# Performance work log

Measured on AMD Instinct MI355X. Metric: run time of the kernel, lower is better.

The kernel has to match this reference:

```python
import jax, jax.numpy as jnp
import numpy as np

D_MODEL = 1024
NUM_HEADS = 16
D_KEY = D_MODEL // NUM_HEADS


def setup_inputs() -> dict:
    key = jax.random.key(0)
    ks = jax.random.split(key, 9)
    B, S = 2, 2048
    s = 1.0 / np.sqrt(D_MODEL)
    return {
        "x": jax.random.normal(ks[0], (B, S, D_MODEL), dtype=jnp.float32),
        "W_q": jax.random.normal(ks[1], (D_MODEL, D_MODEL), dtype=jnp.float32) * s,
        "b_q": jnp.zeros((D_MODEL,), dtype=jnp.float32),
        "W_k": jax.random.normal(ks[2], (D_MODEL, D_MODEL), dtype=jnp.float32) * s,
        "b_k": jnp.zeros((D_MODEL,), dtype=jnp.float32),
        "W_v": jax.random.normal(ks[3], (D_MODEL, D_MODEL), dtype=jnp.float32) * s,
        "b_v": jnp.zeros((D_MODEL,), dtype=jnp.float32),
        "W_o": jax.random.normal(ks[4], (D_MODEL, D_MODEL), dtype=jnp.float32) * s,
        "b_o": jnp.zeros((D_MODEL,), dtype=jnp.float32),
    }


def reference(x, W_q, b_q, W_k, b_k, W_v, b_v, W_o, b_o):
    B, S, _ = x.shape
    # Linear projections (torch nn.Linear: x @ W.T + b; here W stored as [in, out])
    Q = x @ W_q + b_q
    K = x @ W_k + b_k
    V = x @ W_v + b_v
    # [B, S, H, dk] -> [B, H, S, dk]
    def split_heads(t):
        return t.reshape(B, S, NUM_HEADS, D_KEY).transpose(0, 2, 1, 3)
    Q, K, V = split_heads(Q), split_heads(K), split_heads(V)
    scale = 1.0 / np.sqrt(D_KEY).astype(np.float32)
    logits = jnp.einsum("bhqd,bhkd->bhqk", Q, K) * scale  # [B,H,S,S]
    weights = jax.nn.softmax(logits, axis=-1)
    ctx = jnp.einsum("bhqk,bhkd->bhqd", weights, V)       # [B,H,S,dk]
    concat = ctx.transpose(0, 2, 1, 3).reshape(B, S, D_MODEL)
    return concat @ W_o + b_o
```

## Files before the change

### kernel.cpp

```cpp
#include <hip/hip_runtime.h>
#include <cstdint>
#include <cstddef>

#define SEQ   2048
#define NH    16
#define DK    64
#define DM    1024
#define MTOT  4096
#define QSCALE (0.125f * 1.44269504088896f)

typedef __attribute__((ext_vector_type(8))) short           short8;
typedef __attribute__((ext_vector_type(8))) unsigned short  ushort8;
typedef __attribute__((ext_vector_type(4))) unsigned short  ushort4v;
typedef __attribute__((ext_vector_type(2))) unsigned int    uint2v;
typedef __attribute__((ext_vector_type(4))) unsigned int    uint4v;
typedef __attribute__((ext_vector_type(4))) float           float4v;
typedef unsigned short u16;
typedef unsigned int   u32;

__device__ inline float4v mfma16(short8 a, short8 b, float4v c) {
    return __builtin_amdgcn_mfma_f32_16x16x32_bf16(a, b, c, 0, 0, 0);
}
__device__ inline u16 f2bf(float f) {
    u32 u = __float_as_uint(f);
    u += 0x7fffu + ((u >> 16) & 1u);
    return (u16)(u >> 16);
}
__device__ inline u32 pkbf(float a, float b) {
    u32 r;
    asm("v_cvt_pk_bf16_f32 %0, %1, %2" : "=v"(r) : "v"(a), "v"(b));
    return r;
}
__device__ inline float ex2(float x) {
    float r;
    asm("v_exp_f32 %0, %1" : "=v"(r) : "v"(x));
    return r;
}
__device__ inline void pl32swap(u32& a, u32& b) {
    asm("v_permlane32_swap_b32 %0, %1" : "+v"(a), "+v"(b));
}
__device__ inline void pl16swap(u32& a, u32& b) {
    asm("v_permlane16_swap_b32 %0, %1" : "+v"(a), "+v"(b));
}
__device__ inline void gld16(const void* g, void* lds) {
    __builtin_amdgcn_global_load_lds(
        (const __attribute__((address_space(1))) u32*)g,
        (__attribute__((address_space(3))) u32*)lds, 16, 0, 0);
}

__global__ __launch_bounds__(256)
void prep(const float* __restrict__ x, u16* __restrict__ xb,
          const float* __restrict__ W0, const float* __restrict__ W1,
          const float* __restrict__ W2, const float* __restrict__ W3,
          u16* __restrict__ T0, u16* __restrict__ T1,
          u16* __restrict__ T2, u16* __restrict__ T3)
{
    __shared__ u16 t[64][68];
    if (blockIdx.x < 2048) {
        const int i = blockIdx.x * 256 + threadIdx.x;
        const float4v a = ((const float4v*)x)[2 * i];
        const float4v b = ((const float4v*)x)[2 * i + 1];
        ushort8 o;
        #pragma unroll
        for (int j = 0; j < 4; j++) { o[j] = f2bf(a[j]); o[4 + j] = f2bf(b[j]); }
        ((ushort8*)xb)[i] = o;
        return;
    }
    const int bi = blockIdx.x - 2048;
    const int bx = bi & 15, by = (bi >> 4) & 15, bz = bi >> 8;
    const float* W; u16* T;
    switch (bz) {
        case 0: W = W0; T = T0; break;
        case 1: W = W1; T = T1; break;
        case 2: W = W2; T = T2; break;
        default: W = W3; T = T3; break;
    }
    const int n0 = bx * 64, k0 = by * 64;
    const int r  = threadIdx.x >> 4;
    const int c4 = (threadIdx.x & 15) * 4;
    #pragma unroll
    for (int i = 0; i < 4; i++) {
        float4v v = *(const float4v*)&W[(size_t)(k0 + r + i * 16) * DM + n0 + c4];
        #pragma unroll
        for (int j = 0; j < 4; j++) t[r + i * 16][c4 + j] = f2bf(v[j]);
    }
    __syncthreads();
    #pragma unroll
    for (int i = 0; i < 4; i++) {
        const int rr = r + i * 16;
        ushort4v o;
        #pragma unroll
        for (int j = 0; j < 4; j++) o[j] = t[c4 + j][rr];
        *(ushort4v*)&T[(size_t)(n0 + rr) * DM + k0 + c4] = o;
    }
}

template<int TM, int BN, int MODE>
__global__ __launch_bounds__(512)
void gemm_bt(const u16* __restrict__ A, const u16* __restrict__ WT,
             const float* __restrict__ bq, const float* __restrict__ bk,
             const float* __restrict__ bv,
             void* __restrict__ out0, u16* __restrict__ outK, u16* __restrict__ outV)
{
    constexpr int NT = 512;
    constexpr int MF = TM / 32;
    constexpr int NF = BN / 64;
    __shared__ u16 Al[2][TM][64];
    __shared__ u16 Bl[2][BN][64];
    const int tid  = threadIdx.x;
    const int lane = tid & 63, w = tid >> 6;
    const int quad = lane >> 4, l16 = lane & 15;

    const int nxb  = gridDim.x;
    const int wgid = blockIdx.y * nxb + blockIdx.x;
    const int per  = (nxb * gridDim.y) >> 3;
    const int nl   = (wgid & 7) * per + (wgid >> 3);
    const int n0 = (nl % nxb) * BN, m0 = (nl / nxb) * TM;

    const int wm = (w >> 2) * (TM / 2);
    const int wn = (w & 3) * (BN / 4);

    float4v acc[MF][NF] = {};

    auto STAGE = [&](int k0, int buf) {
        #pragma unroll
        for (int j = 0; j < TM * 8 / NT; j++) {
            const int c = j * NT + tid;
            const int row = c >> 3, kc = c & 7;
            gld16(A + (size_t)(m0 + row) * DM + k0 + ((kc ^ (row & 7)) * 8),
                  &Al[buf][0][0] + (size_t)(j * NT + w * 64) * 8);
        }
        #pragma unroll
        for (int j = 0; j < BN * 8 / NT; j++) {
            const int c = j * NT + tid;
            const int row = c >> 3, kc = c & 7;
            gld16(WT + (size_t)(n0 + row) * DM + k0 + ((kc ^ (row & 7)) * 8),
                  &Bl[buf][0][0] + (size_t)(j * NT + w * 64) * 8);
        }
    };

    STAGE(0, 0);
    for (int ks = 0; ks < DM / 64; ++ks) {
        const int buf = ks & 1;
        __syncthreads();
        if (ks + 1 < DM / 64) STAGE((ks + 1) * 64, buf ^ 1);
        #pragma unroll
        for (int u = 0; u < 2; u++) {
            short8 af[MF], bf[NF];
            #pragma unroll
            for (int mi = 0; mi < MF; mi++) {
                const int row = wm + mi * 16 + l16;
                af[mi] = *(const short8*)&Al[buf][row][((4 * u + quad) ^ (row & 7)) * 8];
            }
            #pragma unroll
            for (int ni = 0; ni < NF; ni++) {
                const int row = wn + ni * 16 + l16;
                bf[ni] = *(const short8*)&Bl[buf][row][((4 * u + quad) ^ (row & 7)) * 8];
            }
            __builtin_amdgcn_s_setprio(1);
            #pragma unroll
            for (int mi = 0; mi < MF; mi++)
                #pragma unroll
                for (int ni = 0; ni < NF; ni++)
                    acc[mi][ni] = mfma16(af[mi], bf[ni], acc[mi][ni]);
            __builtin_amdgcn_s_setprio(0);
        }
    }

    if constexpr (MODE == 0) {
        float* out = (float*)out0;
        #pragma unroll
        for (int ni = 0; ni < NF; ni++) {
            const int col = n0 + wn + ni * 16 + l16;
            const float bb = bq[col];
            #pragma unroll
            for (int mi = 0; mi < MF; mi++)
                #pragma unroll
                for (int r = 0; r < 4; r++) {
                    const int row = m0 + wm + mi * 16 + quad * 4 + r;
                    out[(size_t)row * DM + col] = acc[mi][ni][r] + bb;
                }
        }
    } else {
        #pragma unroll
        for (int ni = 0; ni < NF; ni++) {
            const int colg = n0 + wn + ni * 16 + l16;
            const int seg  = colg >> 10;
            u16* outp = (seg == 0) ? (u16*)out0 : (seg == 1 ? outK : outV);
            const float* bias = (seg == 0) ? bq : (seg == 1 ? bk : bv);
            const int col = colg & 1023;
            const float bb = bias[col];
            const int h = col >> 6, d = col & 63;
            if (seg < 2) {
                const float scl = (seg == 0) ? QSCALE : 1.0f;
                #pragma unroll
                for (int mi = 0; mi < MF; mi++)
                    #pragma unroll
                    for (int r = 0; r < 4; r++) {
                        const int row = m0 + wm + mi * 16 + quad * 4 + r;
                        const int b = row >> 11, s = row & (SEQ - 1);
                        outp[(((size_t)(b * NH + h) * SEQ + s) << 6) + d] =
                            f2bf((acc[mi][ni][r] + bb) * scl);
                    }
            } else {
                #pragma unroll
                for (int mi = 0; mi < MF; mi++) {
                    const int row0 = m0 + wm + mi * 16 + quad * 4;
                    const int b = row0 >> 11, s = row0 & (SEQ - 1);
                    uint2v pv;
                    pv[0] = pkbf(acc[mi][ni][0] + bb, acc[mi][ni][1] + bb);
                    pv[1] = pkbf(acc[mi][ni][2] + bb, acc[mi][ni][3] + bb);
                    *(uint2v*)&outp[(((size_t)((b * NH + h) * DK + d)) << 11) + s] = pv;
                }
            }
        }
    }
}

__global__ __launch_bounds__(512, 4)
void attn_kernel(const u16* __restrict__ Q, const u16* __restrict__ K,
                 const u16* __restrict__ VT, u16* __restrict__ Ctx)
{
    __shared__ __align__(16) u16 pool[32768];

    const int tid  = threadIdx.x;
    const int lane = tid & 63, w = tid >> 6;
    const int wq = w & 3, wgrp = w >> 2;
    const int quad = lane >> 4, l16 = lane & 15;

    const int wgid = blockIdx.y * 16 + blockIdx.x;
    const int nlin = (wgid & 7) * 64 + (wgid >> 3);
    const int qt = nlin & 15;
    const int bh = nlin >> 4;
    const size_t head = (size_t)bh * SEQ * DK;

    short8 qf[2][2];
    #pragma unroll
    for (int g = 0; g < 2; g++) {
        const size_t qrow = head + (size_t)(qt * 128 + wq * 32 + g * 16 + l16) * DK;
        qf[g][0] = *(const short8*)(Q + qrow + quad * 8);
        qf[g][1] = *(const short8*)(Q + qrow + 32 + quad * 8);
    }

    float4v acc[2][4] = {};
    float l_part[2] = {0.f, 0.f};

    const int rK = tid >> 3, cK = tid & 7;
    const int sV = (tid >> 8) & 1;
    const int dV = (tid >> 2) & 63, cV = tid & 3;
    const int sVk = (dV & 3) ^ ((dV >> 2) & 3);
    const u16* const Kg = K  + head + (size_t)rK * DK + (cK ^ (rK & 7)) * 8;
    const u16* const Vg = VT + head + (size_t)dV * SEQ + sV * 32 + (cV ^ sVk) * 8;
    u16* const Kdst = pool + tid * 8;
    u16* const Vdst = pool + 16384 + tid * 8;

    auto STAGE = [&](int tile, int buf) {
        const size_t ko = (size_t)tile * 64 * DK;
        const size_t vo = (size_t)tile * 64;
        gld16(Kg + ko,                      Kdst + buf * 8192);
        gld16(Kg + ko + (size_t)1024 * DK,  Kdst + buf * 8192 + 4096);
        gld16(Vg + vo,                      Vdst + buf * 8192);
        gld16(Vg + vo + 1024,               Vdst + buf * 8192 + 4096);
    };

    auto QKSTEP = [&](int buf, int sub, float4v z[2][2]) {
        short8 kf[2][2];
        #pragma unroll
        for (int t = 0; t < 2; t++) {
            const int row = t * 16 + l16;
            const u16* kb = pool + buf * 8192 + wgrp * 4096 + (sub * 32 + row) * 64;
            kf[t][0] = *(const short8*)(kb + (quad ^ (row & 7)) * 8);
            kf[t][1] = *(const short8*)(kb + ((4 + quad) ^ (row & 7)) * 8);
        }
        __builtin_amdgcn_s_setprio(1);
        #pragma unroll
        for (int t = 0; t < 2; t++)
            #pragma unroll
            for (int g = 0; g < 2; g++) {
                float4v zz = {};
                zz = mfma16(kf[t][0], qf[g][0], zz);
                zz = mfma16(kf[t][1], qf[g][1], zz);
                z[t][g] = zz;
            }
        __builtin_amdgcn_s_setprio(0);
    };

    auto SMPACK = [&](float4v zp[2][2], short8 pf[2]) {
        #pragma unroll
        for (int g = 0; g < 2; g++) {
            float p[2][4];
            #pragma unroll
            for (int t = 0; t < 2; t++) {
                p[t][0] = ex2(zp[t][g][0]); p[t][1] = ex2(zp[t][g][1]);
                p[t][2] = ex2(zp[t][g][2]); p[t][3] = ex2(zp[t][g][3]);
                l_part[g] += (p[t][0] + p[t][1]) + (p[t][2] + p[t][3]);
            }
            u32 A = pkbf(p[0][0], p[0][1]);
            u32 B = pkbf(p[0][2], p[0][3]);
            u32 C = pkbf(p[1][0], p[1][1]);
            u32 D = pkbf(p[1][2], p[1][3]);
            pl32swap(A, C); pl16swap(A, C);
            pl32swap(B, D); pl16swap(B, D);
            uint4v pw; pw[0] = A; pw[1] = B; pw[2] = C; pw[3] = D;
            pf[g] = __builtin_bit_cast(short8, pw);
        }
    };

    auto PVSTEP = [&](int buf, int sub, short8 pf[2]) {
        __builtin_amdgcn_s_setprio(1);
        #pragma unroll
        for (int t = 0; t < 4; t++) {
            const int d = t * 16 + l16;
            const u16* vb = pool + 16384 + buf * 8192 + wgrp * 4096
                          + sub * 2048 + d * 32;
            const short8 vf =
                *(const short8*)(vb + (quad ^ ((d & 3) ^ ((d >> 2) & 3))) * 8);
            acc[0][t] = mfma16(vf, pf[0], acc[0][t]);
            acc[1][t] = mfma16(vf, pf[1], acc[1][t]);
        }
        __builtin_amdgcn_s_setprio(0);
    };

    STAGE(0, 0);
    for (int it = 0; it < 16; ++it) {
        const int buf = it & 1;
        __syncthreads();
        if (it + 1 < 16) STAGE(it + 1, buf ^ 1);
        float4v z0[2][2], z1[2][2];
        QKSTEP(buf, 0, z0);
        QKSTEP(buf, 1, z1);
        short8 pf[2];
        SMPACK(z0, pf);
        PVSTEP(buf, 0, pf);
        SMPACK(z1, pf);
        PVSTEP(buf, 1, pf);
    }

    #pragma unroll
    for (int g = 0; g < 2; g++) {
        l_part[g] += __shfl_xor(l_part[g], 16);
        l_part[g] += __shfl_xor(l_part[g], 32);
    }

    float* const Xlp = (float*)pool;
    #define XL(a, b, c) Xlp[(((a) * 64 + (b)) * 17) + (c)]
    float ltot[2];
    #pragma unroll
    for (int p = 0; p < 2; p++) {
        __syncthreads();
        if (wgrp == 1) {
            #pragma unroll
            for (int g = 0; g < 2; g++)
                #pragma unroll
                for (int tt = 0; tt < 2; tt++)
                    #pragma unroll
                    for (int r = 0; r < 4; r++)
                        XL(wq, lane, g * 8 + tt * 4 + r) = acc[g][2 * p + tt][r];
            XL(wq, lane, 16) = l_part[p];
        }
        __syncthreads();
        if (wgrp == 0) {
            #pragma unroll
            for (int g = 0; g < 2; g++)
                #pragma unroll
                for (int tt = 0; tt < 2; tt++)
                    #pragma unroll
                    for (int r = 0; r < 4; r++)
                        acc[g][2 * p + tt][r] += XL(wq, lane, g * 8 + tt * 4 + r);
            ltot[p] = l_part[p] + XL(wq, lane, 16);
        }
    }
    #undef XL

    if (wgrp == 0) {
        const int b = bh >> 4, h = bh & 15;
        #pragma unroll
        for (int g = 0; g < 2; g++) {
            const float rl = 1.0f / ltot[g];
            const int s = qt * 128 + wq * 32 + g * 16 + l16;
            u16* dst = Ctx + (size_t)(b * SEQ + s) * DM + h * 64 + quad * 4;
            #pragma unroll
            for (int t = 0; t < 4; t++) {
                uint2v ov;
                ov[0] = pkbf(acc[g][t][0] * rl, acc[g][t][1] * rl);
                ov[1] = pkbf(acc[g][t][2] * rl, acc[g][t][3] * rl);
                *(uint2v*)&dst[t * 16] = ov;
            }
        }
    }
}

extern "C" void kernel_launch(void* const* d_in, const int* in_sizes, int n_in,
                              void* d_out, int out_size, void* d_ws, size_t ws_size,
                              hipStream_t stream)
{
    const float* x   = (const float*)d_in[0];
    const float* W_q = (const float*)d_in[1];
    const float* b_q = (const float*)d_in[2];
    const float* W_k = (const float*)d_in[3];
    const float* b_k = (const float*)d_in[4];
    const float* W_v = (const float*)d_in[5];
    const float* b_v = (const float*)d_in[6];
    const float* W_o = (const float*)d_in[7];
    const float* b_o = (const float*)d_in[8];

    u16* xb  = (u16*)d_ws;
    u16* WT  = xb + (size_t)MTOT * DM;
    u16* WTo = WT + (size_t)3 * DM * DM;
    u16* VTb = WTo + (size_t)DM * DM;
    u16* Cb  = xb;
    u16* Qb  = (u16*)d_out;
    u16* Kb  = Qb + (size_t)MTOT * DM;

    prep<<<3072, 256, 0, stream>>>(x, xb, W_q, W_k, W_v, W_o,
                                   WT, WT + (size_t)DM * DM,
                                   WT + (size_t)2 * DM * DM, WTo);
    gemm_bt<128, 192, 1><<<dim3(16, 32), 512, 0, stream>>>(
        xb, WT, b_q, b_k, b_v, Qb, Kb, VTb);
    attn_kernel<<<dim3(SEQ / 128, 2 * NH), 512, 0, stream>>>(Qb, Kb, VTb, Cb);
    gemm_bt<64, 128, 0><<<dim3(8, 64), 512, 0, stream>>>(
        Cb, WTo, b_o, nullptr, nullptr, (float*)d_out, nullptr, nullptr);
}
```

Measured before the change: 174.7 us.

## Load V fragments directly from global into registers instead of via LDS

Removes V staging through shared memory. Each lane now loads its V^T fragments straight from global memory into registers at the top of each iteration, and the LDS pool is halved to hold only K tiles. The aim is to cut LDS traffic and footprint, possibly raising occupancy. In exchange, V loads are issued synchronously per iteration with no async double buffering, so the MFMA chain may stall on global memory latency. Each wave group also reads its V rows with small per-lane accesses.

```diff
diff --git a/kernel.cpp b/kernel.cpp
--- a/kernel.cpp
+++ b/kernel.cpp
@@ -221,7 +221,7 @@
 void attn_kernel(const u16* __restrict__ Q, const u16* __restrict__ K,
                  const u16* __restrict__ VT, u16* __restrict__ Ctx)
 {
-    __shared__ __align__(16) u16 pool[32768];
+    __shared__ __align__(16) u16 pool[16384];
 
     const int tid  = threadIdx.x;
     const int lane = tid & 63, w = tid >> 6;
@@ -246,21 +246,18 @@
     float l_part[2] = {0.f, 0.f};
 
     const int rK = tid >> 3, cK = tid & 7;
-    const int sV = (tid >> 8) & 1;
-    const int dV = (tid >> 2) & 63, cV = tid & 3;
-    const int sVk = (dV & 3) ^ ((dV >> 2) & 3);
-    const u16* const Kg = K  + head + (size_t)rK * DK + (cK ^ (rK & 7)) * 8;
-    const u16* const Vg = VT + head + (size_t)dV * SEQ + sV * 32 + (cV ^ sVk) * 8;
+    const u16* const Kg = K + head + (size_t)rK * DK + (cK ^ (rK & 7)) * 8;
     u16* const Kdst = pool + tid * 8;
-    u16* const Vdst = pool + 16384 + tid * 8;
+
+    const u16* Vt[4];
+    #pragma unroll
+    for (int t = 0; t < 4; t++)
+        Vt[t] = VT + head + (size_t)(t * 16 + l16) * SEQ + wgrp * 1024 + quad * 8;
 
     auto STAGE = [&](int tile, int buf) {
         const size_t ko = (size_t)tile * 64 * DK;
-        const size_t vo = (size_t)tile * 64;
         gld16(Kg + ko,                      Kdst + buf * 8192);
         gld16(Kg + ko + (size_t)1024 * DK,  Kdst + buf * 8192 + 4096);
-        gld16(Vg + vo,                      Vdst + buf * 8192);
-        gld16(Vg + vo + 1024,               Vdst + buf * 8192 + 4096);
     };
 
     auto QKSTEP = [&](int buf, int sub, float4v z[2][2]) {
@@ -306,17 +303,12 @@
         }
     };
 
-    auto PVSTEP = [&](int buf, int sub, short8 pf[2]) {
+    auto PVSTEP = [&](const short8 vf[4], short8 pf[2]) {
         __builtin_amdgcn_s_setprio(1);
         #pragma unroll
         for (int t = 0; t < 4; t++) {
-            const int d = t * 16 + l16;
-            const u16* vb = pool + 16384 + buf * 8192 + wgrp * 4096
-                          + sub * 2048 + d * 32;
-            const short8 vf =
-                *(const short8*)(vb + (quad ^ ((d & 3) ^ ((d >> 2) & 3))) * 8);
-            acc[0][t] = mfma16(vf, pf[0], acc[0][t]);
-            acc[1][t] = mfma16(vf, pf[1], acc[1][t]);
+            acc[0][t] = mfma16(vf[t], pf[0], acc[0][t]);
+            acc[1][t] = mfma16(vf[t], pf[1], acc[1][t]);
         }
         __builtin_amdgcn_s_setprio(0);
     };
@@ -325,15 +317,21 @@
     for (int it = 0; it < 16; ++it) {
         const int buf = it & 1;
         __syncthreads();
+        short8 vf0[4], vf1[4];
+        #pragma unroll
+        for (int t = 0; t < 4; t++) {
+            vf0[t] = *(const short8*)(Vt[t] + it * 64);
+            vf1[t] = *(const short8*)(Vt[t] + it * 64 + 32);
+        }
         if (it + 1 < 16) STAGE(it + 1, buf ^ 1);
         float4v z0[2][2], z1[2][2];
         QKSTEP(buf, 0, z0);
         QKSTEP(buf, 1, z1);
         short8 pf[2];
         SMPACK(z0, pf);
-        PVSTEP(buf, 0, pf);
+        PVSTEP(vf0, pf);
         SMPACK(z1, pf);
-        PVSTEP(buf, 1, pf);
+        PVSTEP(vf1, pf);
     }
 
     #pragma unroll
```

After: 231.3 us. 32.4% more time.
